# Kernel tuning notes

Measured on AMD Instinct MI355X. Metric: run time of the kernel, lower is better.

The kernel has to match this reference:

```python
import jax, jax.numpy as jnp
import numpy as np

B, S, E = 2, 2048, 2048
H, D = 16, 128  # num_heads, head_dim = E // H


def setup_inputs() -> dict:
    key = jax.random.key(0)
    ks = jax.random.split(key, 5)
    hidden_states = jax.random.normal(ks[0], (B, S, E), dtype=jnp.float32) * 0.02
    wq = jax.random.normal(ks[1], (E, E), dtype=jnp.float32) * 0.02
    wk = jax.random.normal(ks[2], (E, E), dtype=jnp.float32) * 0.02
    wv = jax.random.normal(ks[3], (E, E), dtype=jnp.float32) * 0.02
    wo = jax.random.normal(ks[4], (E, E), dtype=jnp.float32) * 0.02
    bo = jnp.zeros((E,), dtype=jnp.float32)
    return {"hidden_states": hidden_states, "wq": wq, "wk": wk, "wv": wv, "wo": wo, "bo": bo}


def _split_heads(x):
    # [B, S, E] -> [B, H, S, D]
    return x.reshape(B, S, H, D).transpose(0, 2, 1, 3)


def reference(hidden_states, wq, wk, wv, wo, bo):
    q = _split_heads(hidden_states @ wq)  # [B,H,S,D]
    k = _split_heads(hidden_states @ wk)
    v = _split_heads(hidden_states @ wv)

    # GPT-Neo: no 1/sqrt(d) scaling; scores computed in fp32
    attn_weights = jnp.einsum("bhqd,bhkd->bhqk", q.astype(jnp.float32), k.astype(jnp.float32))

    causal_mask = jnp.tril(jnp.ones((S, S), dtype=bool))  # bias[:, :, :S, :S]
    # Faithful quirk: masked positions get the GLOBAL MIN of attn_weights, not -inf
    mask_value = jnp.min(attn_weights)
    attn_weights = jnp.where(causal_mask, attn_weights, mask_value)

    attn_weights = jax.nn.softmax(attn_weights, axis=-1).astype(v.dtype)
    attn_output = jnp.einsum("bhqk,bhkd->bhqd", attn_weights, v)  # [B,H,S,D]

    # merge heads: [B,H,S,D] -> [B,S,E]
    attn_output = attn_output.transpose(0, 2, 1, 3).reshape(B, S, E)
    attn_output = attn_output @ wo + bo
    return attn_output
```

## Files before the change

### kernel.cpp

```cpp
#include <hip/hip_runtime.h>

typedef unsigned short u16;
typedef unsigned int   u32;
typedef __attribute__((ext_vector_type(4))) float f32x4;
typedef __attribute__((ext_vector_type(4))) u32   u32x4;
typedef __attribute__((ext_vector_type(8))) __bf16 bf16x8;

#define S_LEN 2048
#define EMB   2048
#define NH    16
#define HD    128
#define NBH   32
#define MTOT  4096
#define NBMIN 512

__device__ __forceinline__ u16 f2bf(float f) {
    u32 u = __float_as_uint(f);
    return (u16)((u + 0x7FFFu + ((u >> 16) & 1u)) >> 16);
}
__device__ __forceinline__ float bf2f(u16 v) {
    return __uint_as_float(((u32)v) << 16);
}
__device__ __forceinline__ bf16x8 ld_frag(const u16* p) {
    return __builtin_bit_cast(bf16x8, *(const u32x4*)p);
}
__device__ __forceinline__ void gld_lds16(const void* g, void* l) {
    __builtin_amdgcn_global_load_lds(
        (__attribute__((address_space(1))) void*)(g),
        (__attribute__((address_space(3))) void*)(l), 16, 0, 0);
}

__global__ __launch_bounds__(256) void cast_x_kernel(
    const float* __restrict__ X, u16* __restrict__ Xb)
{
    const size_t i = ((size_t)blockIdx.x * 256 + threadIdx.x) * 8;
    float4 a = *(const float4*)&X[i];
    float4 b = *(const float4*)&X[i + 4];
    u32x4 o;
    o.x = (u32)f2bf(a.x) | ((u32)f2bf(a.y) << 16);
    o.y = (u32)f2bf(a.z) | ((u32)f2bf(a.w) << 16);
    o.z = (u32)f2bf(b.x) | ((u32)f2bf(b.y) << 16);
    o.w = (u32)f2bf(b.z) | ((u32)f2bf(b.w) << 16);
    *(u32x4*)&Xb[i] = o;
}

__global__ __launch_bounds__(256) void transpose_cast_w_kernel(
    const float* __restrict__ W0, const float* __restrict__ W1,
    const float* __restrict__ W2, const float* __restrict__ W3,
    u16* __restrict__ T0, u16* __restrict__ T1,
    u16* __restrict__ T2, u16* __restrict__ T3)
{
    __shared__ float Ls[64][68];
    const int t = threadIdx.x;
    const int n0 = blockIdx.x * 64, k0 = blockIdx.y * 64;
    const int z = blockIdx.z;
    const float* __restrict__ W = (z == 0) ? W0 : (z == 1) ? W1 : (z == 2) ? W2 : W3;
    u16* __restrict__ T = (z == 0) ? T0 : (z == 1) ? T1 : (z == 2) ? T2 : T3;

#pragma unroll
    for (int p = 0; p < 4; ++p) {
        const int r = (t >> 4) + 16 * p;
        const int c = (t & 15) * 4;
        *(float4*)&Ls[r][c] = *(const float4*)&W[(size_t)(k0 + r) * EMB + n0 + c];
    }
    __syncthreads();
    const int nl = t >> 2, q = t & 3;
    u32 pk[8];
#pragma unroll
    for (int j = 0; j < 8; ++j) {
        u16 lo = f2bf(Ls[q * 16 + 2 * j][nl]);
        u16 hi = f2bf(Ls[q * 16 + 2 * j + 1][nl]);
        pk[j] = (u32)lo | ((u32)hi << 16);
    }
    u32x4 o0 = {pk[0], pk[1], pk[2], pk[3]};
    u32x4 o1 = {pk[4], pk[5], pk[6], pk[7]};
    u16* dst = &T[(size_t)(n0 + nl) * EMB + k0 + q * 16];
    *(u32x4*)&dst[0] = o0;
    *(u32x4*)&dst[8] = o1;
}

__global__ __launch_bounds__(256) void transpose_v_kernel(
    const u16* __restrict__ V, u16* __restrict__ Vt)
{
    __shared__ u16 Ls[64][72];
    const int t = threadIdx.x;
    const int s0 = blockIdx.x * 64, d0 = blockIdx.y * 64, bh = blockIdx.z;
    const u16* __restrict__ src0 = V + ((size_t)bh * S_LEN) * HD;
    {
        const int r = t >> 2, c0 = (t & 3) * 16;
        const u16* src = &src0[(size_t)(s0 + r) * HD + d0 + c0];
        *(u32x4*)&Ls[r][c0]     = *(const u32x4*)&src[0];
        *(u32x4*)&Ls[r][c0 + 8] = *(const u32x4*)&src[8];
    }
    __syncthreads();
    const int dl = t >> 2, q = t & 3;
    u32 pk[8];
#pragma unroll
    for (int j = 0; j < 8; ++j) {
        u16 lo = Ls[q * 16 + 2 * j][dl];
        u16 hi = Ls[q * 16 + 2 * j + 1][dl];
        pk[j] = (u32)lo | ((u32)hi << 16);
    }
    u32x4 o0 = {pk[0], pk[1], pk[2], pk[3]};
    u32x4 o1 = {pk[4], pk[5], pk[6], pk[7]};
    u16* dst = &Vt[((size_t)bh * HD + d0 + dl) * S_LEN + s0 + q * 16];
    *(u32x4*)&dst[0] = o0;
    *(u32x4*)&dst[8] = o1;
}

__global__ __launch_bounds__(256) void gemm_qkv_mfma(
    const u16* __restrict__ Xb,
    const u16* __restrict__ Wtq, const u16* __restrict__ Wtk,
    const u16* __restrict__ Wtv,
    u16* __restrict__ Qo, u16* __restrict__ Ko, u16* __restrict__ Vo)
{
    __shared__ __attribute__((aligned(16))) u16 As[128 * 32];
    __shared__ __attribute__((aligned(16))) u16 Bs[128 * 32];
    const int t = threadIdx.x;
    const int w = t >> 6, lane = t & 63;
    const int wy = w >> 1, wx = w & 1;
    const int n0 = blockIdx.x * 128, m0 = blockIdx.y * 128;
    const int z = blockIdx.z;
    const u16* __restrict__ Wt = (z == 0) ? Wtq : (z == 1) ? Wtk : Wtv;
    u16* __restrict__ O = (z == 0) ? Qo : (z == 1) ? Ko : Vo;

    const int srow = lane >> 2, scol = (lane & 3) * 8;
    const u16* Ag = &Xb[(size_t)(m0 + w * 32 + srow) * EMB + scol];
    const u16* Bg = &Wt[(size_t)(n0 + w * 32 + srow) * EMB + scol];
    u16* Al0 = &As[(w * 32) * 32];
    u16* Al1 = &As[(w * 32 + 16) * 32];
    u16* Bl0 = &Bs[(w * 32) * 32];
    u16* Bl1 = &Bs[(w * 32 + 16) * 32];

    const int fm = lane & 15, fk = (lane >> 4) * 8;
    f32x4 acc[4][4];
#pragma unroll
    for (int i = 0; i < 4; ++i)
#pragma unroll
        for (int j = 0; j < 4; ++j) acc[i][j] = (f32x4)0.0f;

    for (int k0 = 0; k0 < EMB; k0 += 32) {
        __syncthreads();
        gld_lds16(Ag + k0, Al0);
        gld_lds16(Ag + 16 * EMB + k0, Al1);
        gld_lds16(Bg + k0, Bl0);
        gld_lds16(Bg + 16 * EMB + k0, Bl1);
        __syncthreads();
        bf16x8 af[4], bfr[4];
#pragma unroll
        for (int mi = 0; mi < 4; ++mi)
            af[mi] = ld_frag(&As[(64 * wy + 16 * mi + fm) * 32 + fk]);
#pragma unroll
        for (int ni = 0; ni < 4; ++ni)
            bfr[ni] = ld_frag(&Bs[(64 * wx + 16 * ni + fm) * 32 + fk]);
#pragma unroll
        for (int mi = 0; mi < 4; ++mi)
#pragma unroll
            for (int ni = 0; ni < 4; ++ni)
                acc[mi][ni] = __builtin_amdgcn_mfma_f32_16x16x32_bf16(
                    af[mi], bfr[ni], acc[mi][ni], 0, 0, 0);
    }

    const int q4 = (lane >> 4) * 4;
#pragma unroll
    for (int mi = 0; mi < 4; ++mi)
#pragma unroll
        for (int ni = 0; ni < 4; ++ni) {
            const int n = n0 + 64 * wx + 16 * ni + (lane & 15);
            const int h = n >> 7, d = n & 127;
#pragma unroll
            for (int r = 0; r < 4; ++r) {
                const int m = m0 + 64 * wy + 16 * mi + q4 + r;
                const int bb = m >> 11, s = m & 2047;
                O[(((size_t)(bb * NH + h) * S_LEN) + s) * HD + d] = f2bf(acc[mi][ni][r]);
            }
        }
}

__global__ __launch_bounds__(256) void gemm_out_mfma(
    const u16* __restrict__ Ab, const u16* __restrict__ Wto,
    const float* __restrict__ bias, float* __restrict__ Out)
{
    __shared__ __attribute__((aligned(16))) u16 As[128 * 32];
    __shared__ __attribute__((aligned(16))) u16 Bs[128 * 32];
    const int t = threadIdx.x;
    const int w = t >> 6, lane = t & 63;
    const int wy = w >> 1, wx = w & 1;
    const int n0 = blockIdx.x * 128, m0 = blockIdx.y * 128;

    const int srow = lane >> 2, scol = (lane & 3) * 8;
    const u16* Ag = &Ab[(size_t)(m0 + w * 32 + srow) * EMB + scol];
    const u16* Bg = &Wto[(size_t)(n0 + w * 32 + srow) * EMB + scol];
    u16* Al0 = &As[(w * 32) * 32];
    u16* Al1 = &As[(w * 32 + 16) * 32];
    u16* Bl0 = &Bs[(w * 32) * 32];
    u16* Bl1 = &Bs[(w * 32 + 16) * 32];

    const int fm = lane & 15, fk = (lane >> 4) * 8;
    f32x4 acc[4][4];
#pragma unroll
    for (int i = 0; i < 4; ++i)
#pragma unroll
        for (int j = 0; j < 4; ++j) acc[i][j] = (f32x4)0.0f;

    for (int k0 = 0; k0 < EMB; k0 += 32) {
        __syncthreads();
        gld_lds16(Ag + k0, Al0);
        gld_lds16(Ag + 16 * EMB + k0, Al1);
        gld_lds16(Bg + k0, Bl0);
        gld_lds16(Bg + 16 * EMB + k0, Bl1);
        __syncthreads();
        bf16x8 af[4], bfr[4];
#pragma unroll
        for (int mi = 0; mi < 4; ++mi)
            af[mi] = ld_frag(&As[(64 * wy + 16 * mi + fm) * 32 + fk]);
#pragma unroll
        for (int ni = 0; ni < 4; ++ni)
            bfr[ni] = ld_frag(&Bs[(64 * wx + 16 * ni + fm) * 32 + fk]);
#pragma unroll
        for (int mi = 0; mi < 4; ++mi)
#pragma unroll
            for (int ni = 0; ni < 4; ++ni)
                acc[mi][ni] = __builtin_amdgcn_mfma_f32_16x16x32_bf16(
                    af[mi], bfr[ni], acc[mi][ni], 0, 0, 0);
    }

    const int q4 = (lane >> 4) * 4;
#pragma unroll
    for (int mi = 0; mi < 4; ++mi)
#pragma unroll
        for (int ni = 0; ni < 4; ++ni) {
            const int n = n0 + 64 * wx + 16 * ni + (lane & 15);
            const float bv = bias[n];
#pragma unroll
            for (int r = 0; r < 4; ++r) {
                const int m = m0 + 64 * wy + 16 * mi + q4 + r;
                Out[(size_t)m * EMB + n] = acc[mi][ni][r] + bv;
            }
        }
}

__global__ __launch_bounds__(256) void reduce_min_kernel(
    const float* __restrict__ bm, float* __restrict__ minval)
{
    __shared__ float sm[256];
    const int t = threadIdx.x;
    float m = 3.0e38f;
    for (int i = t; i < NBMIN; i += 256) m = fminf(m, bm[i]);
    sm[t] = m;
    __syncthreads();
    for (int sft = 128; sft > 0; sft >>= 1) {
        if (t < sft) sm[t] = fminf(sm[t], sm[t + sft]);
        __syncthreads();
    }
    if (t == 0) minval[0] = sm[0];
}

__global__ __launch_bounds__(128) void vchunk_sum_kernel(
    const u16* __restrict__ V, float* __restrict__ csum)
{
    const int chunk = blockIdx.x, bh = blockIdx.y, d = threadIdx.x;
    const u16* vb = V + ((size_t)bh * S_LEN + chunk * 64) * HD + d;
    float s = 0.0f;
    for (int r = 0; r < 64; ++r) s += bf2f(vb[(size_t)r * HD]);
    csum[((size_t)bh * 32 + chunk) * HD + d] = s;
}

__global__ __launch_bounds__(128) void vchunk_suffix_kernel(
    const float* __restrict__ csum, float* __restrict__ csuf)
{
    const int bh = blockIdx.x, d = threadIdx.x;
    float run = 0.0f;
    for (int c = 31; c >= 0; --c) {
        const size_t idx = ((size_t)bh * 32 + c) * HD + d;
        csuf[idx] = run;
        run += csum[idx];
    }
}

__global__ __launch_bounds__(128) void vsuffix_kernel(
    const u16* __restrict__ V, const float* __restrict__ csuf,
    u16* __restrict__ vsuf)
{
    const int chunk = blockIdx.x, bh = blockIdx.y, d = threadIdx.x;
    float run = csuf[((size_t)bh * 32 + chunk) * HD + d];
    const size_t base = ((size_t)bh * S_LEN + chunk * 64) * HD + d;
    for (int r = 63; r >= 0; --r) {
        vsuf[base + (size_t)r * HD] = f2bf(run);
        run += bf2f(V[base + (size_t)r * HD]);
    }
}

__global__ __launch_bounds__(256) void attn_mfma(
    const u16* __restrict__ Q, const u16* __restrict__ K,
    const u16* __restrict__ Vt,
    u16* __restrict__ pacc0, u16* __restrict__ pacc1,
    float* __restrict__ den_p, float* __restrict__ blockmin)
{
    __shared__ __attribute__((aligned(16))) u16 Ps[128 * 136];
    __shared__ __attribute__((aligned(16))) u16 Cs[2][128 * 64];
    __shared__ float den_l[2][128];
    __shared__ float smn[256];

    const int t = threadIdx.x;
    const int w = t >> 6, lane = t & 63;
    const int wy = w >> 1, wx = w & 1;

    const int d_id = blockIdx.y * 16 + blockIdx.x;
    const int f_log = (d_id & 7) * 64 + (d_id >> 3);
    const int pp = (f_log & 15) >> 1, hpar = f_log & 1;
    const int bh = f_log >> 4;
    const int b = bh >> 4, h = bh & 15;

    const u16* __restrict__ Kg  = K + (size_t)bh * S_LEN * HD;
    const u16* __restrict__ Vtg = Vt + (size_t)bh * HD * S_LEN;
    u16* __restrict__ pacc = hpar ? pacc1 : pacc0;

    const int srow8 = lane >> 3;
    const int scol  = ((lane & 7) ^ srow8) * 8;
    const int fm = lane & 15, fk = (lane >> 4) * 8;
    const int key = (fm & 7) * 8;
    const int q4 = (lane >> 4) * 4;

#define STAGE_K(b_, j0_, h_) do { \
        const u16* g_ = &Kg[(size_t)((j0_) + w * 32 + srow8) * HD + (h_) * 64 + scol]; \
        u16* l_ = &Cs[b_][(w * 32) * 64]; \
        gld_lds16(g_,           l_); \
        gld_lds16(g_ + 8 * HD,  l_ + 8 * 64); \
        gld_lds16(g_ + 16 * HD, l_ + 16 * 64); \
        gld_lds16(g_ + 24 * HD, l_ + 24 * 64); } while (0)
#define STAGE_V(b_, j0_, h_) do { \
        const u16* g_ = &Vtg[(size_t)(w * 32 + srow8) * S_LEN + (j0_) + (h_) * 64 + scol]; \
        u16* l_ = &Cs[b_][(w * 32) * 64]; \
        gld_lds16(g_,              l_); \
        gld_lds16(g_ + 8 * S_LEN,  l_ + 8 * 64); \
        gld_lds16(g_ + 16 * S_LEN, l_ + 16 * 64); \
        gld_lds16(g_ + 24 * S_LEN, l_ + 24 * 64); } while (0)

    float mn = 3.0e38f;
    int c = 0;

    STAGE_K(0, hpar * 128, 0);
    __syncthreads();

    for (int pass = 0; pass < 2; ++pass) {
        const int qt = pass ? (15 - pp) : pp;
        const int i0 = qt * 128;
        const u16* __restrict__ Qg = Q + ((size_t)bh * S_LEN + i0) * HD;

        bf16x8 af[4][4];
#pragma unroll
        for (int mi = 0; mi < 4; ++mi)
#pragma unroll
            for (int dk = 0; dk < 4; ++dk)
                af[mi][dk] = ld_frag(
                    &Qg[(size_t)(64 * wy + 16 * mi + fm) * HD + dk * 32 + fk]);

        f32x4 oacc[4][4];
#pragma unroll
        for (int i = 0; i < 4; ++i)
#pragma unroll
            for (int j = 0; j < 4; ++j) oacc[i][j] = (f32x4)0.0f;
        float den[4][4] = {};

        for (int ji = 0; ji < 8; ++ji) {
            const int jt = hpar + 2 * ji;
            const int j0 = jt * 128;
            const bool causal = (jt <= qt);
            const bool hn = (ji < 7) || (pass == 0);
            const int nj0 = (ji < 7) ? (jt + 2) * 128 : hpar * 128;

            f32x4 sacc[4][4];
#pragma unroll
            for (int i = 0; i < 4; ++i)
#pragma unroll
                for (int j = 0; j < 4; ++j) sacc[i][j] = (f32x4)0.0f;

            STAGE_K(c ^ 1, j0, 1);
#pragma unroll
            for (int dk2 = 0; dk2 < 2; ++dk2) {
                bf16x8 bfr[4];
#pragma unroll
                for (int ni = 0; ni < 4; ++ni)
                    bfr[ni] = ld_frag(&Cs[c][(64 * wx + 16 * ni + fm) * 64
                                             + ((dk2 * 32 + fk) ^ key)]);
#pragma unroll
                for (int mi = 0; mi < 4; ++mi)
#pragma unroll
                    for (int ni = 0; ni < 4; ++ni)
                        sacc[mi][ni] = __builtin_amdgcn_mfma_f32_16x16x32_bf16(
                            af[mi][dk2], bfr[ni], sacc[mi][ni], 0, 0, 0);
            }
            __syncthreads();
            c ^= 1;

            if (causal)      STAGE_V(c ^ 1, j0, 0);
            else if (hn)     STAGE_K(c ^ 1, nj0, 0);
#pragma unroll
            for (int dk2 = 0; dk2 < 2; ++dk2) {
                bf16x8 bfr[4];
#pragma unroll
                for (int ni = 0; ni < 4; ++ni)
                    bfr[ni] = ld_frag(&Cs[c][(64 * wx + 16 * ni + fm) * 64
                                             + ((dk2 * 32 + fk) ^ key)]);
#pragma unroll
                for (int mi = 0; mi < 4; ++mi)
#pragma unroll
                    for (int ni = 0; ni < 4; ++ni)
                        sacc[mi][ni] = __builtin_amdgcn_mfma_f32_16x16x32_bf16(
                            af[mi][2 + dk2], bfr[ni], sacc[mi][ni], 0, 0, 0);
            }
            if (causal) {
                const bool dg = (jt == qt);
#pragma unroll
                for (int mi = 0; mi < 4; ++mi) {
                    const int rbase = 64 * wy + 16 * mi + q4;
#pragma unroll
                    for (int ni = 0; ni < 4; ++ni) {
                        const int cl = 64 * wx + 16 * ni + fm;
                        const int jg = j0 + cl;
#pragma unroll
                        for (int r = 0; r < 4; ++r) {
                            const float s = sacc[mi][ni][r];
                            mn = fminf(mn, s);
                            float e = __expf(s);
                            if (dg && jg > i0 + rbase + r) e = 0.0f;
                            den[mi][r] += e;
                            Ps[(rbase + r) * 136 + cl] = f2bf(e);
                        }
                    }
                }
            } else {
#pragma unroll
                for (int mi = 0; mi < 4; ++mi)
#pragma unroll
                    for (int ni = 0; ni < 4; ++ni)
#pragma unroll
                        for (int r = 0; r < 4; ++r)
                            mn = fminf(mn, sacc[mi][ni][r]);
            }
            __syncthreads();
            c ^= 1;

            if (causal) {
                STAGE_V(c ^ 1, j0, 1);
#pragma unroll
                for (int sk2 = 0; sk2 < 2; ++sk2) {
                    const int sk = sk2;
                    bf16x8 pa[4], pb[4];
#pragma unroll
                    for (int mi = 0; mi < 4; ++mi)
                        pa[mi] = ld_frag(&Ps[(64 * wy + 16 * mi + fm) * 136
                                             + sk * 32 + fk]);
#pragma unroll
                    for (int ni = 0; ni < 4; ++ni)
                        pb[ni] = ld_frag(&Cs[c][(64 * wx + 16 * ni + fm) * 64
                                                + ((sk2 * 32 + fk) ^ key)]);
#pragma unroll
                    for (int mi = 0; mi < 4; ++mi)
#pragma unroll
                        for (int ni = 0; ni < 4; ++ni)
                            oacc[mi][ni] = __builtin_amdgcn_mfma_f32_16x16x32_bf16(
                                pa[mi], pb[ni], oacc[mi][ni], 0, 0, 0);
                }
                __syncthreads();
                c ^= 1;

                if (hn) STAGE_K(c ^ 1, nj0, 0);
#pragma unroll
                for (int sk2 = 0; sk2 < 2; ++sk2) {
                    const int sk = 2 + sk2;
                    bf16x8 pa[4], pb[4];
#pragma unroll
                    for (int mi = 0; mi < 4; ++mi)
                        pa[mi] = ld_frag(&Ps[(64 * wy + 16 * mi + fm) * 136
                                             + sk * 32 + fk]);
#pragma unroll
                    for (int ni = 0; ni < 4; ++ni)
                        pb[ni] = ld_frag(&Cs[c][(64 * wx + 16 * ni + fm) * 64
                                                + ((sk2 * 32 + fk) ^ key)]);
#pragma unroll
                    for (int mi = 0; mi < 4; ++mi)
#pragma unroll
                        for (int ni = 0; ni < 4; ++ni)
                            oacc[mi][ni] = __builtin_amdgcn_mfma_f32_16x16x32_bf16(
                                pa[mi], pb[ni], oacc[mi][ni], 0, 0, 0);
                }
                __syncthreads();
                c ^= 1;
            }
        }

#pragma unroll
        for (int mi = 0; mi < 4; ++mi)
#pragma unroll
            for (int r = 0; r < 4; ++r) {
                float v = den[mi][r];
                v += __shfl_xor(v, 1, 64);
                v += __shfl_xor(v, 2, 64);
                v += __shfl_xor(v, 4, 64);
                v += __shfl_xor(v, 8, 64);
                den[mi][r] = v;
            }
        __syncthreads();
        if ((lane & 15) == 0) {
#pragma unroll
            for (int mi = 0; mi < 4; ++mi)
#pragma unroll
                for (int r = 0; r < 4; ++r)
                    den_l[wx][64 * wy + 16 * mi + q4 + r] = den[mi][r];
        }
        __syncthreads();
        if (t < 128)
            den_p[((size_t)hpar * NBH + bh) * S_LEN + i0 + t] =
                den_l[0][t] + den_l[1][t];

#pragma unroll
        for (int mi = 0; mi < 4; ++mi)
#pragma unroll
            for (int ni = 0; ni < 4; ++ni) {
                const int d = 64 * wx + 16 * ni + fm;
#pragma unroll
                for (int r = 0; r < 4; ++r) {
                    const int row = 64 * wy + 16 * mi + q4 + r;
                    pacc[((size_t)b * S_LEN + i0 + row) * EMB + h * HD + d] =
                        f2bf(oacc[mi][ni][r]);
                }
            }
        __syncthreads();
    }

    smn[t] = mn;
    __syncthreads();
    for (int sft = 128; sft > 0; sft >>= 1) {
        if (t < sft) smn[t] = fminf(smn[t], smn[t + sft]);
        __syncthreads();
    }
    if (t == 0) blockmin[d_id] = smn[0];

#undef STAGE_K
#undef STAGE_V
}

__global__ __launch_bounds__(256) void finalize_kernel(
    u16* __restrict__ outm, const u16* __restrict__ pacc1,
    const u16* __restrict__ vsuf, const float* __restrict__ den_p,
    const float* __restrict__ minval)
{
    const size_t i = ((size_t)blockIdx.x * 256 + threadIdx.x) * 8;
    const int e = (int)(i & (EMB - 1));
    const int m = (int)(i / EMB);
    const int b = m >> 11, s = m & 2047;
    const int hh = e >> 7, d = e & 127;
    const int bh = b * NH + hh;
    const float em = __expf(minval[0]);
    const float den = den_p[(size_t)bh * S_LEN + s]
                    + den_p[((size_t)NBH + bh) * S_LEN + s]
                    + (float)(S_LEN - 1 - s) * em;
    const float inv = 1.0f / den;
    u32x4 a = *(const u32x4*)&outm[i];
    u32x4 cc = *(const u32x4*)&pacc1[i];
    u32x4 vv = *(const u32x4*)&vsuf[((size_t)bh * S_LEN + s) * HD + d];
    const u16* pa = (const u16*)&a;
    const u16* pc = (const u16*)&cc;
    const u16* pv = (const u16*)&vv;
    u16 ov[8];
#pragma unroll
    for (int j = 0; j < 8; ++j) {
        const float v = bf2f(pa[j]) + bf2f(pc[j]) + em * bf2f(pv[j]);
        ov[j] = f2bf(v * inv);
    }
    *(u32x4*)&outm[i] = *(const u32x4*)ov;
}

extern "C" void kernel_launch(void* const* d_in, const int* in_sizes, int n_in,
                              void* d_out, int out_size, void* d_ws, size_t ws_size,
                              hipStream_t stream)
{
    (void)in_sizes; (void)n_in; (void)out_size; (void)ws_size;
    const float* hs = (const float*)d_in[0];
    const float* wq = (const float*)d_in[1];
    const float* wk = (const float*)d_in[2];
    const float* wv = (const float*)d_in[3];
    const float* wo = (const float*)d_in[4];
    const float* bo = (const float*)d_in[5];
    float* out = (float*)d_out;

    char* p = (char*)d_ws;
    const size_t TS = (size_t)NBH * S_LEN * HD;
    u16* Xb   = (u16*)p; p += (size_t)MTOT * EMB * 2;
    u16* Wtq  = (u16*)p; p += (size_t)EMB * EMB * 2;
    u16* Wtk  = (u16*)p; p += (size_t)EMB * EMB * 2;
    u16* Wtv  = (u16*)p; p += (size_t)EMB * EMB * 2;
    u16* Wto  = (u16*)p; p += (size_t)EMB * EMB * 2;
    u16* Qb   = (u16*)p; p += TS * 2;
    u16* Kb   = (u16*)p; p += TS * 2;
    u16* Vb   = (u16*)p; p += TS * 2;
    u16* Vtb  = (u16*)p; p += TS * 2;
    u16* outm = (u16*)p; p += (size_t)MTOT * EMB * 2;
    u16* vsuf = (u16*)p; p += TS * 2;
    float* csum     = (float*)p; p += (size_t)NBH * 32 * HD * 4;
    float* csuf     = (float*)p; p += (size_t)NBH * 32 * HD * 4;
    float* blockmin = (float*)p; p += 1024 * 4;
    float* minval   = (float*)p; p += 64;
    float* den_p    = (float*)p; p += (size_t)2 * NBH * S_LEN * 4;
    u16* pacc1 = Xb;

    cast_x_kernel<<<4096, 256, 0, stream>>>(hs, Xb);
    transpose_cast_w_kernel<<<dim3(32, 32, 4), 256, 0, stream>>>(
        wq, wk, wv, wo, Wtq, Wtk, Wtv, Wto);

    gemm_qkv_mfma<<<dim3(EMB / 128, MTOT / 128, 3), 256, 0, stream>>>(
        Xb, Wtq, Wtk, Wtv, Qb, Kb, Vb);

    transpose_v_kernel<<<dim3(32, 2, NBH), 256, 0, stream>>>(Vb, Vtb);
    vchunk_sum_kernel<<<dim3(32, NBH), 128, 0, stream>>>(Vb, csum);
    vchunk_suffix_kernel<<<NBH, 128, 0, stream>>>(csum, csuf);
    vsuffix_kernel<<<dim3(32, NBH), 128, 0, stream>>>(Vb, csuf, vsuf);

    attn_mfma<<<dim3(16, NBH), 256, 0, stream>>>(
        Qb, Kb, Vtb, outm, pacc1, den_p, blockmin);

    reduce_min_kernel<<<1, 256, 0, stream>>>(blockmin, minval);

    finalize_kernel<<<(MTOT * EMB / 8) / 256, 256, 0, stream>>>(
        outm, pacc1, vsuf, den_p, minval);

    gemm_out_mfma<<<dim3(EMB / 128, MTOT / 128), 256, 0, stream>>>(
        outm, Wto, bo, out);
}
```

Measured before the change: 444.4 us.

## Double GEMM K-tile to 64 with XOR-swizzled LDS layout

Both projection GEMMs now stage 64-wide K slices per iteration instead of 32, which halves the number of barrier pairs per tile. The shared-memory layout is XOR-swizzled by row so that fragment reads from 128-byte rows avoid bank conflicts. The cost is doubled LDS use per block, which may lower occupancy, and the staging loads and reads depend on the swizzle index maths being correct.

```diff
diff --git a/kernel.cpp b/kernel.cpp
--- a/kernel.cpp
+++ b/kernel.cpp
@@ -114,8 +114,8 @@
     const u16* __restrict__ Wtv,
     u16* __restrict__ Qo, u16* __restrict__ Ko, u16* __restrict__ Vo)
 {
-    __shared__ __attribute__((aligned(16))) u16 As[128 * 32];
-    __shared__ __attribute__((aligned(16))) u16 Bs[128 * 32];
+    __shared__ __attribute__((aligned(16))) u16 As[128 * 64];
+    __shared__ __attribute__((aligned(16))) u16 Bs[128 * 64];
     const int t = threadIdx.x;
     const int w = t >> 6, lane = t & 63;
     const int wy = w >> 1, wx = w & 1;
@@ -124,41 +124,51 @@
     const u16* __restrict__ Wt = (z == 0) ? Wtq : (z == 1) ? Wtk : Wtv;
     u16* __restrict__ O = (z == 0) ? Qo : (z == 1) ? Ko : Vo;
 
-    const int srow = lane >> 2, scol = (lane & 3) * 8;
-    const u16* Ag = &Xb[(size_t)(m0 + w * 32 + srow) * EMB + scol];
-    const u16* Bg = &Wt[(size_t)(n0 + w * 32 + srow) * EMB + scol];
-    u16* Al0 = &As[(w * 32) * 32];
-    u16* Al1 = &As[(w * 32 + 16) * 32];
-    u16* Bl0 = &Bs[(w * 32) * 32];
-    u16* Bl1 = &Bs[(w * 32 + 16) * 32];
-
+    const int srow8 = lane >> 3;
+    const int scol  = ((lane & 7) ^ srow8) * 8;
     const int fm = lane & 15, fk = (lane >> 4) * 8;
+    const int key = (fm & 7) * 8;
+
+    const u16* Ag = &Xb[(size_t)(m0 + w * 32 + srow8) * EMB + scol];
+    const u16* Bg = &Wt[(size_t)(n0 + w * 32 + srow8) * EMB + scol];
+    u16* const Al = &As[(w * 32) * 64];
+    u16* const Bl = &Bs[(w * 32) * 64];
+
     f32x4 acc[4][4];
 #pragma unroll
     for (int i = 0; i < 4; ++i)
 #pragma unroll
         for (int j = 0; j < 4; ++j) acc[i][j] = (f32x4)0.0f;
 
-    for (int k0 = 0; k0 < EMB; k0 += 32) {
-        __syncthreads();
-        gld_lds16(Ag + k0, Al0);
-        gld_lds16(Ag + 16 * EMB + k0, Al1);
-        gld_lds16(Bg + k0, Bl0);
-        gld_lds16(Bg + 16 * EMB + k0, Bl1);
-        __syncthreads();
-        bf16x8 af[4], bfr[4];
-#pragma unroll
-        for (int mi = 0; mi < 4; ++mi)
-            af[mi] = ld_frag(&As[(64 * wy + 16 * mi + fm) * 32 + fk]);
-#pragma unroll
-        for (int ni = 0; ni < 4; ++ni)
-            bfr[ni] = ld_frag(&Bs[(64 * wx + 16 * ni + fm) * 32 + fk]);
-#pragma unroll
-        for (int mi = 0; mi < 4; ++mi)
+    for (int k0 = 0; k0 < EMB; k0 += 64) {
+        __syncthreads();
+        gld_lds16(Ag + k0,               Al);
+        gld_lds16(Ag + k0 + 8 * EMB,     Al + 8 * 64);
+        gld_lds16(Ag + k0 + 16 * EMB,    Al + 16 * 64);
+        gld_lds16(Ag + k0 + 24 * EMB,    Al + 24 * 64);
+        gld_lds16(Bg + k0,               Bl);
+        gld_lds16(Bg + k0 + 8 * EMB,     Bl + 8 * 64);
+        gld_lds16(Bg + k0 + 16 * EMB,    Bl + 16 * 64);
+        gld_lds16(Bg + k0 + 24 * EMB,    Bl + 24 * 64);
+        __syncthreads();
+#pragma unroll
+        for (int dk2 = 0; dk2 < 2; ++dk2) {
+            bf16x8 af[4], bfr[4];
+#pragma unroll
+            for (int mi = 0; mi < 4; ++mi)
+                af[mi] = ld_frag(&As[(64 * wy + 16 * mi + fm) * 64
+                                     + ((dk2 * 32 + fk) ^ key)]);
 #pragma unroll
             for (int ni = 0; ni < 4; ++ni)
-                acc[mi][ni] = __builtin_amdgcn_mfma_f32_16x16x32_bf16(
-                    af[mi], bfr[ni], acc[mi][ni], 0, 0, 0);
+                bfr[ni] = ld_frag(&Bs[(64 * wx + 16 * ni + fm) * 64
+                                      + ((dk2 * 32 + fk) ^ key)]);
+#pragma unroll
+            for (int mi = 0; mi < 4; ++mi)
+#pragma unroll
+                for (int ni = 0; ni < 4; ++ni)
+                    acc[mi][ni] = __builtin_amdgcn_mfma_f32_16x16x32_bf16(
+                        af[mi], bfr[ni], acc[mi][ni], 0, 0, 0);
+        }
     }
 
     const int q4 = (lane >> 4) * 4;
@@ -181,48 +191,58 @@
     const u16* __restrict__ Ab, const u16* __restrict__ Wto,
     const float* __restrict__ bias, float* __restrict__ Out)
 {
-    __shared__ __attribute__((aligned(16))) u16 As[128 * 32];
-    __shared__ __attribute__((aligned(16))) u16 Bs[128 * 32];
+    __shared__ __attribute__((aligned(16))) u16 As[128 * 64];
+    __shared__ __attribute__((aligned(16))) u16 Bs[128 * 64];
     const int t = threadIdx.x;
     const int w = t >> 6, lane = t & 63;
     const int wy = w >> 1, wx = w & 1;
     const int n0 = blockIdx.x * 128, m0 = blockIdx.y * 128;
 
-    const int srow = lane >> 2, scol = (lane & 3) * 8;
-    const u16* Ag = &Ab[(size_t)(m0 + w * 32 + srow) * EMB + scol];
-    const u16* Bg = &Wto[(size_t)(n0 + w * 32 + srow) * EMB + scol];
-    u16* Al0 = &As[(w * 32) * 32];
-    u16* Al1 = &As[(w * 32 + 16) * 32];
-    u16* Bl0 = &Bs[(w * 32) * 32];
-    u16* Bl1 = &Bs[(w * 32 + 16) * 32];
-
+    const int srow8 = lane >> 3;
+    const int scol  = ((lane & 7) ^ srow8) * 8;
     const int fm = lane & 15, fk = (lane >> 4) * 8;
+    const int key = (fm & 7) * 8;
+
+    const u16* Ag = &Ab[(size_t)(m0 + w * 32 + srow8) * EMB + scol];
+    const u16* Bg = &Wto[(size_t)(n0 + w * 32 + srow8) * EMB + scol];
+    u16* const Al = &As[(w * 32) * 64];
+    u16* const Bl = &Bs[(w * 32) * 64];
+
     f32x4 acc[4][4];
 #pragma unroll
     for (int i = 0; i < 4; ++i)
 #pragma unroll
         for (int j = 0; j < 4; ++j) acc[i][j] = (f32x4)0.0f;
 
-    for (int k0 = 0; k0 < EMB; k0 += 32) {
-        __syncthreads();
-        gld_lds16(Ag + k0, Al0);
-        gld_lds16(Ag + 16 * EMB + k0, Al1);
-        gld_lds16(Bg + k0, Bl0);
-        gld_lds16(Bg + 16 * EMB + k0, Bl1);
-        __syncthreads();
-        bf16x8 af[4], bfr[4];
-#pragma unroll
-        for (int mi = 0; mi < 4; ++mi)
-            af[mi] = ld_frag(&As[(64 * wy + 16 * mi + fm) * 32 + fk]);
-#pragma unroll
-        for (int ni = 0; ni < 4; ++ni)
-            bfr[ni] = ld_frag(&Bs[(64 * wx + 16 * ni + fm) * 32 + fk]);
-#pragma unroll
-        for (int mi = 0; mi < 4; ++mi)
+    for (int k0 = 0; k0 < EMB; k0 += 64) {
+        __syncthreads();
+        gld_lds16(Ag + k0,               Al);
+        gld_lds16(Ag + k0 + 8 * EMB,     Al + 8 * 64);
+        gld_lds16(Ag + k0 + 16 * EMB,    Al + 16 * 64);
+        gld_lds16(Ag + k0 + 24 * EMB,    Al + 24 * 64);
+        gld_lds16(Bg + k0,               Bl);
+        gld_lds16(Bg + k0 + 8 * EMB,     Bl + 8 * 64);
+        gld_lds16(Bg + k0 + 16 * EMB,    Bl + 16 * 64);
+        gld_lds16(Bg + k0 + 24 * EMB,    Bl + 24 * 64);
+        __syncthreads();
+#pragma unroll
+        for (int dk2 = 0; dk2 < 2; ++dk2) {
+            bf16x8 af[4], bfr[4];
+#pragma unroll
+            for (int mi = 0; mi < 4; ++mi)
+                af[mi] = ld_frag(&As[(64 * wy + 16 * mi + fm) * 64
+                                     + ((dk2 * 32 + fk) ^ key)]);
 #pragma unroll
             for (int ni = 0; ni < 4; ++ni)
-                acc[mi][ni] = __builtin_amdgcn_mfma_f32_16x16x32_bf16(
-                    af[mi], bfr[ni], acc[mi][ni], 0, 0, 0);
+                bfr[ni] = ld_frag(&Bs[(64 * wx + 16 * ni + fm) * 64
+                                      + ((dk2 * 32 + fk) ^ key)]);
+#pragma unroll
+            for (int mi = 0; mi < 4; ++mi)
+#pragma unroll
+                for (int ni = 0; ni < 4; ++ni)
+                    acc[mi][ni] = __builtin_amdgcn_mfma_f32_16x16x32_bf16(
+                        af[mi], bfr[ni], acc[mi][ni], 0, 0, 0);
+        }
     }
 
     const int q4 = (lane >> 4) * 4;
```

Result: no change. 438.3 us (-1.4%).
